# Kernel tuning notes

Measured on AMD Instinct MI355X. Metric: run time of the kernel, lower is better.

The kernel has to match this reference:

```python
import jax, jax.numpy as jnp
import numpy as np

TEMPERATURE = 0.07
NEG_INF = -1e9


def setup_inputs() -> dict:
    key = jax.random.key(0)
    k1, k2, k3, k4, k5 = jax.random.split(key, 5)
    B, L, H = 64, 256, 64
    query_embs = jax.random.normal(k1, (B, L, H), dtype=jnp.float32)
    key_embs = jax.random.normal(k2, (B, L, H), dtype=jnp.float32)
    labels = jax.random.randint(k3, (B,), 0, 2, dtype=jnp.int64)
    q_mask = jax.random.randint(k4, (B, L), 0, 2, dtype=jnp.int32)
    k_mask = jax.random.randint(k5, (B, L), 0, 2, dtype=jnp.int32)
    return {"query_embs": query_embs, "key_embs": key_embs, "labels": labels,
            "q_mask": q_mask, "k_mask": k_mask}


def reference(query_embs, key_embs, labels, q_mask, k_mask):
    # ColBERT-style late interaction over all B x B pairs.
    # sim: (B_q, B_k, Lq, Lk) token-level dot products.
    sim = jnp.einsum('bqh,ckh->bcqk', query_embs, key_embs)
    # Mask out padded key tokens before the max over key positions.
    sim = jnp.where(k_mask[None, :, None, :].astype(bool), sim, NEG_INF)
    maxsim = jnp.max(sim, axis=-1)                      # (B_q, B_k, Lq)
    qm = q_mask[:, None, :].astype(maxsim.dtype)        # (B_q, 1, Lq)
    scores = jnp.sum(maxsim * qm, axis=-1) / TEMPERATURE  # (B_q, B_k)
    # Cross-entropy on rows with labels==1, target = diagonal index.
    logp = jax.nn.log_softmax(scores, axis=-1)
    B = scores.shape[0]
    diag = logp[jnp.arange(B), jnp.arange(B)]           # (B,)
    w = labels.astype(scores.dtype)
    denom = jnp.maximum(jnp.sum(w), 1.0)
    return -jnp.sum(w * diag) / denom
```

## Files before the change

### kernel.cpp

```cpp
#include <hip/hip_runtime.h>
#include <math.h>

#define PB 64
#define PL 256
#define PH 64
#define TEMP 0.07f
#define NEG_INF_F (-1e9f)

#define KSTRIDE 72

typedef short short8 __attribute__((ext_vector_type(8)));
typedef float f32x4 __attribute__((ext_vector_type(4)));

__device__ __forceinline__ unsigned short f32_to_bf16(float f) {
    unsigned int u = __float_as_uint(f);
    u += 0x7FFFu + ((u >> 16) & 1u);
    return (unsigned short)(u >> 16);
}

__global__ void convert_kernel(const float* __restrict__ Q,
                               const float* __restrict__ K,
                               unsigned short* __restrict__ Qb,
                               unsigned short* __restrict__ Kb) {
    const int t = blockIdx.x * blockDim.x + threadIdx.x;
    const int NV4 = (PB * PL * PH) / 4;
    const float4* src;
    unsigned short* dst;
    int i;
    if (t < NV4) { src = (const float4*)Q; dst = Qb; i = t; }
    else         { src = (const float4*)K; dst = Kb; i = t - NV4; }
    float4 v = src[i];
    ushort4 o;
    o.x = f32_to_bf16(v.x); o.y = f32_to_bf16(v.y);
    o.z = f32_to_bf16(v.z); o.w = f32_to_bf16(v.w);
    *(ushort4*)(dst + (size_t)i * 4) = o;
}

__global__ __launch_bounds__(256)
void colbert_scores_mfma(const unsigned short* __restrict__ Qb,
                         const unsigned short* __restrict__ Kb,
                         const int*   __restrict__ qmask,
                         const int*   __restrict__ kmask,
                         float*       __restrict__ scores) {
    const int c = blockIdx.x;
    const int b = blockIdx.y;
    const int tid  = threadIdx.x;
    const int wave = tid >> 6;
    const int lane = tid & 63;
    const int n    = lane & 15;
    const int g    = (lane >> 4) & 3;

    __shared__ __align__(16) unsigned short Ks[PL * KSTRIDE];
    __shared__ int   kmI[PL];
    __shared__ float qmF[PL];
    __shared__ float red[4];

    kmI[tid] = kmask[c * PL + tid];
    qmF[tid] = (float)qmask[b * PL + tid];

    {
        const unsigned short* Kbase = Kb + ((size_t)c * PL) * PH;
        #pragma unroll
        for (int it = 0; it < (PL * PH) / (256 * 8); ++it) {
            int lin = it * 256 + tid;
            int row = lin >> 3;
            int off = lin & 7;
            ushort4 v0 = *(const ushort4*)(Kbase + (size_t)row * PH + off * 8);
            ushort4 v1 = *(const ushort4*)(Kbase + (size_t)row * PH + off * 8 + 4);
            *(ushort4*)(&Ks[row * KSTRIDE + off * 8])     = v0;
            *(ushort4*)(&Ks[row * KSTRIDE + off * 8 + 4]) = v1;
        }
    }

    const int qw0 = wave * 64;
    short8 afrag[4][2];
    {
        const unsigned short* Qrow = Qb + ((size_t)b * PL) * PH;
        #pragma unroll
        for (int rt = 0; rt < 4; ++rt) {
            const unsigned short* p = Qrow + (size_t)(qw0 + rt * 16 + n) * PH + g * 8;
            afrag[rt][0] = *(const short8*)(p);
            afrag[rt][1] = *(const short8*)(p + 32);
        }
    }

    __syncthreads();

    float maxv[4][4];
    #pragma unroll
    for (int rt = 0; rt < 4; ++rt)
        #pragma unroll
        for (int r = 0; r < 4; ++r) maxv[rt][r] = NEG_INF_F;

    for (int ct = 0; ct < 16; ++ct) {
        const int km = kmI[ct * 16 + n];
        const unsigned short* krow = &Ks[(ct * 16 + n) * KSTRIDE + g * 8];
        short8 b0 = *(const short8*)(krow);
        short8 b1 = *(const short8*)(krow + 32);

        f32x4 acc[4];
        #pragma unroll
        for (int rt = 0; rt < 4; ++rt) acc[rt] = (f32x4){0.f, 0.f, 0.f, 0.f};
        #pragma unroll
        for (int rt = 0; rt < 4; ++rt)
            acc[rt] = __builtin_amdgcn_mfma_f32_16x16x32_bf16(afrag[rt][0], b0, acc[rt], 0, 0, 0);
        #pragma unroll
        for (int rt = 0; rt < 4; ++rt)
            acc[rt] = __builtin_amdgcn_mfma_f32_16x16x32_bf16(afrag[rt][1], b1, acc[rt], 0, 0, 0);

        #pragma unroll
        for (int rt = 0; rt < 4; ++rt)
            #pragma unroll
            for (int r = 0; r < 4; ++r) {
                float s = km ? acc[rt][r] : NEG_INF_F;
                maxv[rt][r] = fmaxf(maxv[rt][r], s);
            }
    }

    #pragma unroll
    for (int rt = 0; rt < 4; ++rt)
        #pragma unroll
        for (int r = 0; r < 4; ++r) {
            float mv = maxv[rt][r];
            mv = fmaxf(mv, __shfl_xor(mv, 1, 16));
            mv = fmaxf(mv, __shfl_xor(mv, 2, 16));
            mv = fmaxf(mv, __shfl_xor(mv, 4, 16));
            mv = fmaxf(mv, __shfl_xor(mv, 8, 16));
            maxv[rt][r] = mv;
        }

    float partial = 0.0f;
    if (n == 0) {
        #pragma unroll
        for (int rt = 0; rt < 4; ++rt)
            #pragma unroll
            for (int r = 0; r < 4; ++r) {
                int row = qw0 + rt * 16 + g * 4 + r;
                partial += maxv[rt][r] * qmF[row];
            }
    }
    partial += __shfl_xor(partial, 16, 64);
    partial += __shfl_xor(partial, 32, 64);
    if (lane == 0) red[wave] = partial;
    __syncthreads();
    if (tid == 0) {
        float total = red[0] + red[1] + red[2] + red[3];
        scores[b * PB + c] = total * (1.0f / TEMP);
    }
}

__global__ void finalize_kernel(const float* __restrict__ scores,
                                const int*   __restrict__ labels,
                                float*       __restrict__ out) {
    const int r = threadIdx.x;
    const float* row = scores + r * PB;
    float mx = NEG_INF_F;
    for (int j = 0; j < PB; ++j) mx = fmaxf(mx, row[j]);
    float se = 0.0f;
    for (int j = 0; j < PB; ++j) se += expf(row[j] - mx);
    float logp_diag = row[r] - mx - logf(se);
    float w = (float)labels[r];
    float wd = w * logp_diag;
    #pragma unroll
    for (int off = 32; off >= 1; off >>= 1) {
        wd += __shfl_xor(wd, off, 64);
        w  += __shfl_xor(w,  off, 64);
    }
    if (r == 0) out[0] = -wd / fmaxf(w, 1.0f);
}

extern "C" void kernel_launch(void* const* d_in, const int* in_sizes, int n_in,
                              void* d_out, int out_size, void* d_ws, size_t ws_size,
                              hipStream_t stream) {
    const float* Q      = (const float*)d_in[0];
    const float* K      = (const float*)d_in[1];
    const int*   labels = (const int*)d_in[2];
    const int*   qmask  = (const int*)d_in[3];
    const int*   kmask  = (const int*)d_in[4];
    float*       out    = (float*)d_out;

    char* ws = (char*)d_ws;
    float*          scores = (float*)ws;
    unsigned short* Qb     = (unsigned short*)(ws + 16 * 1024);
    unsigned short* Kb     = (unsigned short*)(ws + 16 * 1024 + 2 * 1024 * 1024);

    const int total_v4 = 2 * (PB * PL * PH) / 4;
    convert_kernel<<<total_v4 / 256, 256, 0, stream>>>(Q, K, Qb, Kb);

    dim3 grid(PB, PB);
    colbert_scores_mfma<<<grid, 256, 0, stream>>>(Qb, Kb, qmask, kmask, scores);
    finalize_kernel<<<1, 64, 0, stream>>>(scores, labels, out);
}
```

Before: 116.2 us.

## Compact unmasked key tokens in prep and skip masked keys in MFMA loop

The prep kernel now packs only the unmasked key rows of each batch into a bf16 slab, zero-pads the slab to a multiple of 16 rows, and records the valid count per batch. The score kernel loads only that compacted slab into LDS using direct global-to-LDS loads and iterates only over the valid key tiles. The per-element mask select is gone: a -1e9 bias in the accumulator covers the partial last tile, and the main loop handles two tiles per iteration. This targets the MFMA and LDS work spent on padded keys, at the cost of a less parallel prep kernel (128 blocks) and data-dependent loop trip counts.

```diff
diff --git a/kernel.cpp b/kernel.cpp
--- a/kernel.cpp
+++ b/kernel.cpp
@@ -8,6 +8,8 @@
 #define NEG_INF_F (-1e9f)
 
 #define KSTRIDE 72
+#define KROWB   (KSTRIDE * 2)
+#define KSLAB   (PL * KSTRIDE)
 
 typedef short short8 __attribute__((ext_vector_type(8)));
 typedef float f32x4 __attribute__((ext_vector_type(4)));
@@ -18,29 +20,69 @@
     return (unsigned short)(u >> 16);
 }
 
-__global__ void convert_kernel(const float* __restrict__ Q,
-                               const float* __restrict__ K,
-                               unsigned short* __restrict__ Qb,
-                               unsigned short* __restrict__ Kb) {
-    const int t = blockIdx.x * blockDim.x + threadIdx.x;
-    const int NV4 = (PB * PL * PH) / 4;
-    const float4* src;
-    unsigned short* dst;
-    int i;
-    if (t < NV4) { src = (const float4*)Q; dst = Qb; i = t; }
-    else         { src = (const float4*)K; dst = Kb; i = t - NV4; }
-    float4 v = src[i];
-    ushort4 o;
-    o.x = f32_to_bf16(v.x); o.y = f32_to_bf16(v.y);
-    o.z = f32_to_bf16(v.z); o.w = f32_to_bf16(v.w);
-    *(ushort4*)(dst + (size_t)i * 4) = o;
+__global__ __launch_bounds__(256)
+void prep_kernel(const float* __restrict__ Q,
+                 const float* __restrict__ K,
+                 const int*   __restrict__ kmask,
+                 unsigned short* __restrict__ Qb,
+                 unsigned short* __restrict__ Kcomp,
+                 int* __restrict__ nvK) {
+    const int tid = threadIdx.x;
+
+    if (blockIdx.x >= PB) {
+        const int b = blockIdx.x - PB;
+        const float4* src = (const float4*)(Q + (size_t)b * PL * PH);
+        unsigned short* dst = Qb + (size_t)b * PL * PH;
+        #pragma unroll
+        for (int it = 0; it < (PL * PH / 4) / 256; ++it) {
+            int i = it * 256 + tid;
+            float4 v = src[i];
+            ushort4 o;
+            o.x = f32_to_bf16(v.x); o.y = f32_to_bf16(v.y);
+            o.z = f32_to_bf16(v.z); o.w = f32_to_bf16(v.w);
+            *(ushort4*)(dst + (size_t)i * 4) = o;
+        }
+        return;
+    }
+
+    const int c    = blockIdx.x;
+    const int lane = tid & 63;
+    const int wave = tid >> 6;
+    __shared__ int posArr[PL];
+    __shared__ int wcnt[4];
+
+    const int km = kmask[c * PL + tid];
+    unsigned long long bal = __ballot(km != 0);
+    int within = __popcll(bal & ((1ull << lane) - 1ull));
+    if (lane == 0) wcnt[wave] = __popcll(bal);
+    __syncthreads();
+    int base = 0;
+    #pragma unroll
+    for (int w = 0; w < 4; ++w) base += (w < wave) ? wcnt[w] : 0;
+    posArr[tid] = km ? (base + within) : -1;
+    const int nv = wcnt[0] + wcnt[1] + wcnt[2] + wcnt[3];
+    __syncthreads();
+
+    unsigned short* slab = Kcomp + (size_t)c * KSLAB;
+    for (int r = wave; r < PL; r += 4) {
+        int p = posArr[r];
+        if (p >= 0) {
+            float v = K[((size_t)c * PL + r) * PH + lane];
+            slab[(size_t)p * KSTRIDE + lane] = f32_to_bf16(v);
+        }
+    }
+    const int rows16 = (nv + 15) & ~15;
+    for (int p = nv + wave; p < rows16; p += 4) {
+        slab[(size_t)p * KSTRIDE + lane] = 0;
+    }
+    if (tid == 0) nvK[c] = nv;
 }
 
 __global__ __launch_bounds__(256)
 void colbert_scores_mfma(const unsigned short* __restrict__ Qb,
-                         const unsigned short* __restrict__ Kb,
+                         const unsigned short* __restrict__ Kcomp,
+                         const int*   __restrict__ nvK,
                          const int*   __restrict__ qmask,
-                         const int*   __restrict__ kmask,
                          float*       __restrict__ scores) {
     const int c = blockIdx.x;
     const int b = blockIdx.y;
@@ -51,24 +93,25 @@
     const int g    = (lane >> 4) & 3;
 
     __shared__ __align__(16) unsigned short Ks[PL * KSTRIDE];
-    __shared__ int   kmI[PL];
     __shared__ float qmF[PL];
     __shared__ float red[4];
 
-    kmI[tid] = kmask[c * PL + tid];
+    const int nv     = nvK[c];
+    const int rows16 = (nv + 15) & ~15;
+    const int nbytes = rows16 * KROWB;
+
     qmF[tid] = (float)qmask[b * PL + tid];
 
     {
-        const unsigned short* Kbase = Kb + ((size_t)c * PL) * PH;
-        #pragma unroll
-        for (int it = 0; it < (PL * PH) / (256 * 8); ++it) {
-            int lin = it * 256 + tid;
-            int row = lin >> 3;
-            int off = lin & 7;
-            ushort4 v0 = *(const ushort4*)(Kbase + (size_t)row * PH + off * 8);
-            ushort4 v1 = *(const ushort4*)(Kbase + (size_t)row * PH + off * 8 + 4);
-            *(ushort4*)(&Ks[row * KSTRIDE + off * 8])     = v0;
-            *(ushort4*)(&Ks[row * KSTRIDE + off * 8 + 4]) = v1;
+        const char* gsrc  = (const char*)(Kcomp + (size_t)c * KSLAB);
+        char*       lbase = (char*)Ks;
+        const int nchunks = (nbytes + 4095) >> 12;
+        for (int it = 0; it < nchunks; ++it) {
+            int off = it * 4096 + tid * 16;
+            __builtin_amdgcn_global_load_lds(
+                (const __attribute__((address_space(1))) unsigned int*)(gsrc + off),
+                (__attribute__((address_space(3)))       unsigned int*)(lbase + off),
+                16, 0, 0);
         }
     }
 
@@ -92,29 +135,74 @@
         #pragma unroll
         for (int r = 0; r < 4; ++r) maxv[rt][r] = NEG_INF_F;
 
-    for (int ct = 0; ct < 16; ++ct) {
-        const int km = kmI[ct * 16 + n];
-        const unsigned short* krow = &Ks[(ct * 16 + n) * KSTRIDE + g * 8];
-        short8 b0 = *(const short8*)(krow);
-        short8 b1 = *(const short8*)(krow + 32);
-
+    const f32x4 ZERO4 = (f32x4){0.f, 0.f, 0.f, 0.f};
+    const int ntFull   = nv >> 4;
+    const int tailCols = nv & 15;
+    const unsigned short* krow0 = &Ks[n * KSTRIDE + g * 8];
+
+    int ct = 0;
+    for (; ct + 1 < ntFull; ct += 2) {
+        const unsigned short* ka = krow0 + ct * 16 * KSTRIDE;
+        short8 kA0 = *(const short8*)(ka);
+        short8 kA1 = *(const short8*)(ka + 32);
+        short8 kB0 = *(const short8*)(ka + 16 * KSTRIDE);
+        short8 kB1 = *(const short8*)(ka + 16 * KSTRIDE + 32);
+
+        f32x4 accA[4], accB[4];
+        #pragma unroll
+        for (int rt = 0; rt < 4; ++rt) {
+            accA[rt] = __builtin_amdgcn_mfma_f32_16x16x32_bf16(afrag[rt][0], kA0, ZERO4, 0, 0, 0);
+            accB[rt] = __builtin_amdgcn_mfma_f32_16x16x32_bf16(afrag[rt][0], kB0, ZERO4, 0, 0, 0);
+        }
+        #pragma unroll
+        for (int rt = 0; rt < 4; ++rt) {
+            accA[rt] = __builtin_amdgcn_mfma_f32_16x16x32_bf16(afrag[rt][1], kA1, accA[rt], 0, 0, 0);
+            accB[rt] = __builtin_amdgcn_mfma_f32_16x16x32_bf16(afrag[rt][1], kB1, accB[rt], 0, 0, 0);
+        }
+        #pragma unroll
+        for (int rt = 0; rt < 4; ++rt)
+            #pragma unroll
+            for (int r = 0; r < 4; ++r)
+                maxv[rt][r] = fmaxf(maxv[rt][r], fmaxf(accA[rt][r], accB[rt][r]));
+    }
+
+    if (ntFull & 1) {
+        const unsigned short* ka = krow0 + ct * 16 * KSTRIDE;
+        short8 k0 = *(const short8*)(ka);
+        short8 k1 = *(const short8*)(ka + 32);
         f32x4 acc[4];
         #pragma unroll
-        for (int rt = 0; rt < 4; ++rt) acc[rt] = (f32x4){0.f, 0.f, 0.f, 0.f};
-        #pragma unroll
-        for (int rt = 0; rt < 4; ++rt)
-            acc[rt] = __builtin_amdgcn_mfma_f32_16x16x32_bf16(afrag[rt][0], b0, acc[rt], 0, 0, 0);
-        #pragma unroll
-        for (int rt = 0; rt < 4; ++rt)
-            acc[rt] = __builtin_amdgcn_mfma_f32_16x16x32_bf16(afrag[rt][1], b1, acc[rt], 0, 0, 0);
-
-        #pragma unroll
-        for (int rt = 0; rt < 4; ++rt)
-            #pragma unroll
-            for (int r = 0; r < 4; ++r) {
-                float s = km ? acc[rt][r] : NEG_INF_F;
-                maxv[rt][r] = fmaxf(maxv[rt][r], s);
-            }
+        for (int rt = 0; rt < 4; ++rt)
+            acc[rt] = __builtin_amdgcn_mfma_f32_16x16x32_bf16(afrag[rt][0], k0, ZERO4, 0, 0, 0);
+        #pragma unroll
+        for (int rt = 0; rt < 4; ++rt)
+            acc[rt] = __builtin_amdgcn_mfma_f32_16x16x32_bf16(afrag[rt][1], k1, acc[rt], 0, 0, 0);
+        #pragma unroll
+        for (int rt = 0; rt < 4; ++rt)
+            #pragma unroll
+            for (int r = 0; r < 4; ++r)
+                maxv[rt][r] = fmaxf(maxv[rt][r], acc[rt][r]);
+        ct++;
+    }
+
+    if (tailCols) {
+        float biasv = (n < tailCols) ? 0.0f : NEG_INF_F;
+        f32x4 BIAS4 = (f32x4){biasv, biasv, biasv, biasv};
+        const unsigned short* ka = krow0 + ct * 16 * KSTRIDE;
+        short8 k0 = *(const short8*)(ka);
+        short8 k1 = *(const short8*)(ka + 32);
+        f32x4 acc[4];
+        #pragma unroll
+        for (int rt = 0; rt < 4; ++rt)
+            acc[rt] = __builtin_amdgcn_mfma_f32_16x16x32_bf16(afrag[rt][0], k0, BIAS4, 0, 0, 0);
+        #pragma unroll
+        for (int rt = 0; rt < 4; ++rt)
+            acc[rt] = __builtin_amdgcn_mfma_f32_16x16x32_bf16(afrag[rt][1], k1, acc[rt], 0, 0, 0);
+        #pragma unroll
+        for (int rt = 0; rt < 4; ++rt)
+            #pragma unroll
+            for (int r = 0; r < 4; ++r)
+                maxv[rt][r] = fmaxf(maxv[rt][r], acc[rt][r]);
     }
 
     #pragma unroll
@@ -182,12 +270,12 @@
     char* ws = (char*)d_ws;
     float*          scores = (float*)ws;
     unsigned short* Qb     = (unsigned short*)(ws + 16 * 1024);
-    unsigned short* Kb     = (unsigned short*)(ws + 16 * 1024 + 2 * 1024 * 1024);
-
-    const int total_v4 = 2 * (PB * PL * PH) / 4;
-    convert_kernel<<<total_v4 / 256, 256, 0, stream>>>(Q, K, Qb, Kb);
+    unsigned short* Kcomp  = (unsigned short*)(ws + 16 * 1024 + 2 * 1024 * 1024);
+    int*            nvK    = (int*)(ws + 16 * 1024 + 2 * 1024 * 1024 + (size_t)PB * KSLAB * 2);
+
+    prep_kernel<<<128, 256, 0, stream>>>(Q, K, kmask, Qb, Kcomp, nvK);
 
     dim3 grid(PB, PB);
-    colbert_scores_mfma<<<grid, 256, 0, stream>>>(Qb, Kb, qmask, kmask, scores);
+    colbert_scores_mfma<<<grid, 256, 0, stream>>>(Qb, Kcomp, nvK, qmask, scores);
     finalize_kernel<<<1, 64, 0, stream>>>(scores, labels, out);
 }
```

After: 116.3 us. About the same (+0.2%).
